# Kernel optimization log

Hardware: AMD Instinct MI355X
Metric: run time of the kernel (lower is better)

Reference implementation:

```python
import jax, jax.numpy as jnp
import numpy as np

B, T, C = 4, 2048, 1024
N_HEAD = 16
HEAD = C // N_HEAD

def setup_inputs() -> dict:
    key = jax.random.key(0)
    ks = jax.random.split(key, 5)
    return {
        "x": jax.random.normal(ks[0], (B, T, C), dtype=jnp.float32),
        "W_attn": jax.random.normal(ks[1], (C, 3 * C), dtype=jnp.float32) * (C ** -0.5),
        "b_attn": jax.random.normal(ks[2], (3 * C,), dtype=jnp.float32) * 0.02,
        "W_proj": jax.random.normal(ks[3], (C, C), dtype=jnp.float32) * (C ** -0.5),
        "b_proj": jax.random.normal(ks[4], (C,), dtype=jnp.float32) * 0.02,
    }

def reference(x, W_attn, b_attn, W_proj, b_proj):
    Bx, Tx, Cx = x.shape
    qkv = x @ W_attn + b_attn  # [B,T,3C]
    q, k, v = jnp.split(qkv, 3, axis=2)
    # [B,T,H,D] -> [B,H,T,D]
    q = q.reshape(Bx, Tx, N_HEAD, HEAD).transpose(0, 2, 1, 3)
    k = k.reshape(Bx, Tx, N_HEAD, HEAD).transpose(0, 2, 1, 3)
    v = v.reshape(Bx, Tx, N_HEAD, HEAD).transpose(0, 2, 1, 3)
    att = jnp.einsum('bhqd,bhkd->bhqk', q, k) * (HEAD ** -0.5)
    causal = jnp.tril(jnp.ones((Tx, Tx), dtype=bool))
    att = jnp.where(causal, att, jnp.float32(-jnp.inf))
    att = jax.nn.softmax(att, axis=-1)
    y = jnp.einsum('bhqk,bhkd->bhqd', att, v)
    y = y.transpose(0, 2, 1, 3).reshape(Bx, Tx, Cx)
    return y @ W_proj + b_proj
```

## Files before the change

kernel.cpp:

```cpp
#include <hip/hip_runtime.h>
#include <stdint.h>

#define NB 4
#define TT 2048
#define CC 1024
#define NH 16
#define DD 64
#define BHH (NB*NH)
#define MROWS (NB*TT)

typedef uint16_t u16;
typedef uint32_t u32;
typedef __bf16 bf16x8 __attribute__((ext_vector_type(8)));
typedef float f32x4 __attribute__((ext_vector_type(4)));
typedef float f32x16 __attribute__((ext_vector_type(16)));

__device__ __forceinline__ u16 f2bf(float f) {
    union { float f; uint32_t u; } v; v.f = f;
    uint32_t u = v.u;
    return (u16)((u + 0x7FFF + ((u >> 16) & 1)) >> 16);
}

__device__ __forceinline__ u32 cvtpk(float lo, float hi) {
    u32 r;
    asm volatile("v_cvt_pk_bf16_f32 %0, %1, %2" : "=v"(r) : "v"(lo), "v"(hi));
    return r;
}

__device__ __forceinline__ void plswap(u32& a, u32& b) {
    asm volatile("v_permlane32_swap_b32 %0, %1" : "+v"(a), "+v"(b));
}

__device__ __forceinline__ bf16x8 mk8(u32 a, u32 b, u32 c, u32 d) {
    union { u32 u[4]; bf16x8 v; } x;
    x.u[0] = a; x.u[1] = b; x.u[2] = c; x.u[3] = d;
    return x.v;
}

__device__ __forceinline__ void gl_lds16(const u16* g, u16* l) {
    __builtin_amdgcn_global_load_lds(
        (const __attribute__((address_space(1))) unsigned int*)g,
        (__attribute__((address_space(3))) unsigned int*)l, 16, 0, 0);
}

__device__ __forceinline__ f32x4 mfma16(bf16x8 a, bf16x8 b, f32x4 c) {
    return __builtin_amdgcn_mfma_f32_16x16x32_bf16(a, b, c, 0, 0, 0);
}
__device__ __forceinline__ f32x16 mfma32(bf16x8 a, bf16x8 b, f32x16 c) {
    return __builtin_amdgcn_mfma_f32_32x32x16_bf16(a, b, c, 0, 0, 0);
}

__global__ __launch_bounds__(256) void k_f2b(const float* __restrict__ in,
                                             u16* __restrict__ out, int n) {
    const int i = (blockIdx.x * 256 + threadIdx.x) * 4;
    if (i >= n) return;
    const float4 v = *(const float4*)(in + i);
    ushort4 o;
    o.x = f2bf(v.x); o.y = f2bf(v.y); o.z = f2bf(v.z); o.w = f2bf(v.w);
    *(ushort4*)(out + i) = o;
}

__global__ __launch_bounds__(256) void k_transpose_cvt(const float* __restrict__ in,
                                                       u16* __restrict__ out,
                                                       int R, int N) {
    __shared__ float t[32][33];
    const int n0 = blockIdx.x * 32, r0 = blockIdx.y * 32;
    const int c  = threadIdx.x & 31, rq = threadIdx.x >> 5;
#pragma unroll
    for (int i = 0; i < 4; ++i) {
        int r = rq + i * 8;
        t[r][c] = in[(r0 + r) * N + n0 + c];
    }
    __syncthreads();
#pragma unroll
    for (int i = 0; i < 4; ++i) {
        int r = rq + i * 8;
        out[(n0 + r) * R + r0 + c] = f2bf(t[c][r]);
    }
}

#define VM8()  do { asm volatile("s_waitcnt vmcnt(8)" ::: "memory"); \
                    __builtin_amdgcn_sched_barrier(0); } while (0)
#define VM0()  do { asm volatile("s_waitcnt vmcnt(0)" ::: "memory"); \
                    __builtin_amdgcn_sched_barrier(0); } while (0)

__device__ __forceinline__ void gemm128v4(const u16* __restrict__ A,
                                          const u16* __restrict__ Bt,
                                          int m0, int n0, f32x4 acc[4][4]) {
    __shared__ __align__(16) u16 As[2][128 * 64];
    __shared__ __align__(16) u16 Bs[2][128 * 64];
    const int tid = threadIdx.x, l = tid & 63, w = tid >> 6;
    const int wr = w >> 1, wc = w & 1;
    const int lr = l & 15, lg = l >> 4;

    auto stage = [&](int kt, int b) {
#pragma unroll
        for (int line = 0; line < 4; ++line) {
            const int s = line * 4096 + tid * 16;
            const int row = s >> 7;
            const int colb = (s & 127) ^ ((row & 7) << 4);
            const int ldsoff = (line * 4096 + w * 1024) >> 1;
            gl_lds16(A  + (size_t)(m0 + row) * 1024 + kt * 64 + (colb >> 1),
                     &As[b][ldsoff]);
            gl_lds16(Bt + (size_t)(n0 + row) * 1024 + kt * 64 + (colb >> 1),
                     &Bs[b][ldsoff]);
        }
    };

    stage(0, 0);
    stage(1, 1);
    VM8();
    __builtin_amdgcn_s_barrier();

    for (int kt = 0; kt < 16; ++kt) {
        const int b = kt & 1;

#pragma unroll
        for (int ks = 0; ks < 2; ++ks) {
            bf16x8 af[4], bf[4];
#pragma unroll
            for (int m = 0; m < 4; ++m) {
                const int row = wr * 64 + m * 16 + lr;
                const int byteC = (ks * 64 + lg * 16) ^ ((row & 7) << 4);
                af[m] = *(const bf16x8*)&As[b][(row * 128 + byteC) >> 1];
            }
#pragma unroll
            for (int n = 0; n < 4; ++n) {
                const int row = wc * 64 + n * 16 + lr;
                const int byteC = (ks * 64 + lg * 16) ^ ((row & 7) << 4);
                bf[n] = *(const bf16x8*)&Bs[b][(row * 128 + byteC) >> 1];
            }
#pragma unroll
            for (int m = 0; m < 4; ++m)
#pragma unroll
                for (int n = 0; n < 4; ++n)
                    acc[m][n] = mfma16(af[m], bf[n], acc[m][n]);
        }

        if (kt == 15) break;

        __builtin_amdgcn_s_barrier();

        if (kt + 2 < 16) {
            stage(kt + 2, b);
            VM8();
        } else {
            VM0();
        }
        __builtin_amdgcn_s_barrier();
    }
}

__global__ __launch_bounds__(256, 2) void k_gemm_qkv(const u16* __restrict__ X,
                                                     const u16* __restrict__ Wt,
                                                     const float* __restrict__ bias,
                                                     u16* __restrict__ Qo,
                                                     u16* __restrict__ Ko,
                                                     u16* __restrict__ Vto) {
    const int id = blockIdx.x;
    const int xcd = id & 7, lid = id >> 3;
    const int lm = lid & 7, ln = lid >> 3;
    const int m0 = (xcd * 8 + lm) * 128;
    const int n0 = ln * 128;

    f32x4 acc[4][4];
#pragma unroll
    for (int m = 0; m < 4; ++m)
#pragma unroll
        for (int n = 0; n < 4; ++n) acc[m][n] = (f32x4){0.f, 0.f, 0.f, 0.f};
    gemm128v4(X, Wt, m0, n0, acc);

    const float C2 = 0.18033688011112042f;
    const int tid = threadIdx.x, l = tid & 63, w = tid >> 6;
    const int wr = w >> 1, wc = w & 1, lr = l & 15, lg = l >> 4;
#pragma unroll
    for (int n = 0; n < 4; ++n) {
        const int c = n0 + wc * 64 + n * 16 + lr;
        const float bv = bias[c];
        const int which = c >> 10, cc = c & 1023, h = cc >> 6, d = cc & 63;
#pragma unroll
        for (int m = 0; m < 4; ++m) {
            const int rbase = m0 + wr * 64 + m * 16 + lg * 4;
#pragma unroll
            for (int j = 0; j < 4; ++j) {
                const int r = rbase + j;
                const int b = r >> 11, t = r & 2047;
                const int bh = b * NH + h;
                const float v = acc[m][n][j] + bv;
                if (which == 0)      Qo[(bh * TT + t) * DD + d] = f2bf(v * C2);
                else if (which == 1) Ko[(bh * TT + t) * DD + d] = f2bf(v);
                else                 Vto[(bh * DD + d) * TT + t] = f2bf(v);
            }
        }
    }
}

__global__ __launch_bounds__(256, 2) void k_gemm_proj(const u16* __restrict__ Yin,
                                                      const u16* __restrict__ Wt,
                                                      const float* __restrict__ bias,
                                                      float* __restrict__ out) {
    const int id = blockIdx.x;
    const int xcd = id & 7, lid = id >> 3;
    const int lm = lid & 7, ln = lid >> 3;
    const int m0 = (xcd * 8 + lm) * 128;
    const int n0 = ln * 128;

    f32x4 acc[4][4];
#pragma unroll
    for (int m = 0; m < 4; ++m)
#pragma unroll
        for (int n = 0; n < 4; ++n) acc[m][n] = (f32x4){0.f, 0.f, 0.f, 0.f};
    gemm128v4(Yin, Wt, m0, n0, acc);

    const int tid = threadIdx.x, l = tid & 63, w = tid >> 6;
    const int wr = w >> 1, wc = w & 1, lr = l & 15, lg = l >> 4;
#pragma unroll
    for (int n = 0; n < 4; ++n) {
        const int c = n0 + wc * 64 + n * 16 + lr;
        const float bv = bias[c];
#pragma unroll
        for (int m = 0; m < 4; ++m) {
            const int rbase = m0 + wr * 64 + m * 16 + lg * 4;
#pragma unroll
            for (int j = 0; j < 4; ++j) {
                const int r = rbase + j;
                out[r * CC + c] = acc[m][n][j] + bv;
            }
        }
    }
}

__global__ __launch_bounds__(256) void k_attn(const u16* __restrict__ Qg_,
                                              const u16* __restrict__ Kg_,
                                              const u16* __restrict__ Vg_,
                                              u16* __restrict__ Y) {
    __shared__ __align__(16) u16 Ks[2][64 * 64];
    __shared__ __align__(16) u16 Vs[2][64 * 64];

    const int id = blockIdx.x;
    const int qi = 15 - (id >> 6);
    const int bh = id & 63;
    const int q0 = qi * 128;
    const u16* Qg = Qg_ + (size_t)bh * TT * DD;
    const u16* Kg = Kg_ + (size_t)bh * TT * DD;
    const u16* Vg = Vg_ + (size_t)bh * DD * TT;
    const int tid = threadIdx.x, l = tid & 63, w = tid >> 6;
    const int lq = l & 31, hi = l >> 5;
    const int qs = q0 + w * 32;

    unsigned dmask = 0;
#pragma unroll
    for (int r = 0; r < 16; ++r) {
        const int kvloc = (r & 3) + 8 * (r >> 2) + 4 * hi;
        if (kvloc > lq) dmask |= (1u << r);
    }

    const u16* qrow = Qg + (qs + lq) * DD + hi * 8;
    bf16x8 qf0 = *(const bf16x8*)(qrow);
    bf16x8 qf1 = *(const bf16x8*)(qrow + 16);
    bf16x8 qf2 = *(const bf16x8*)(qrow + 32);
    bf16x8 qf3 = *(const bf16x8*)(qrow + 48);

    f32x16 o0 = {}, o1 = {};
    float mrun = -1e30f, lrun = 0.f;
    const int nt = 2 * qi + 2;

    auto stage = [&](int t, int b) {
        const int kv0 = t * 64;
#pragma unroll
        for (int iss = 0; iss < 2; ++iss) {
            const int s = iss * 4096 + tid * 16;
            const int row = s >> 7;
            const int colb = (s & 127) ^ ((row & 7) << 4);
            const int ldsoff = (iss * 4096 + w * 1024) >> 1;
            gl_lds16(Kg + (kv0 + row) * DD + (colb >> 1), &Ks[b][ldsoff]);
            gl_lds16(Vg + row * TT + kv0 + (colb >> 1),   &Vs[b][ldsoff]);
        }
    };

    stage(0, 0);
    __syncthreads();

    for (int t = 0; t < nt; ++t) {
        const int b = t & 1;
        if (t + 1 < nt) stage(t + 1, b ^ 1);
        const int kv0 = t * 64;

#pragma unroll
        for (int s = 0; s < 2; ++s) {
            const int kvs = kv0 + 32 * s;
            if (kvs > qs) continue;

            f32x16 st = {};
#pragma unroll
            for (int i = 0; i < 4; ++i) {
                const int row = 32 * s + lq;
                const int byte = (32 * i + 16 * hi) ^ ((row & 7) << 4);
                const bf16x8 kf = *(const bf16x8*)&Ks[b][(row * 128 + byte) >> 1];
                if (i == 0) st = mfma32(kf, qf0, st);
                else if (i == 1) st = mfma32(kf, qf1, st);
                else if (i == 2) st = mfma32(kf, qf2, st);
                else st = mfma32(kf, qf3, st);
            }

            if (kvs == qs) {
#pragma unroll
                for (int r = 0; r < 16; ++r)
                    if ((dmask >> r) & 1) st[r] = -1e30f;
            }

            float mx = st[0];
#pragma unroll
            for (int r = 1; r < 16; ++r) mx = fmaxf(mx, st[r]);
            mx = fmaxf(mx, __shfl_xor(mx, 32));

            if (!__all(mx - mrun <= 8.0f)) {
                const float mn = fmaxf(mrun, mx);
                const float scl = __builtin_amdgcn_exp2f(mrun - mn);
                mrun = mn;
                lrun *= scl;
#pragma unroll
                for (int r = 0; r < 16; ++r) { o0[r] *= scl; o1[r] *= scl; }
            }

            float psum = 0.f;
            u32 pk0, pk1, pk2, pk3, pk4, pk5, pk6, pk7;
            {
                float pa, pb;
                pa = __builtin_amdgcn_exp2f(st[0] - mrun);
                pb = __builtin_amdgcn_exp2f(st[1] - mrun);
                psum += pa + pb; pk0 = cvtpk(pa, pb);
                pa = __builtin_amdgcn_exp2f(st[2] - mrun);
                pb = __builtin_amdgcn_exp2f(st[3] - mrun);
                psum += pa + pb; pk1 = cvtpk(pa, pb);
                pa = __builtin_amdgcn_exp2f(st[4] - mrun);
                pb = __builtin_amdgcn_exp2f(st[5] - mrun);
                psum += pa + pb; pk2 = cvtpk(pa, pb);
                pa = __builtin_amdgcn_exp2f(st[6] - mrun);
                pb = __builtin_amdgcn_exp2f(st[7] - mrun);
                psum += pa + pb; pk3 = cvtpk(pa, pb);
                pa = __builtin_amdgcn_exp2f(st[8] - mrun);
                pb = __builtin_amdgcn_exp2f(st[9] - mrun);
                psum += pa + pb; pk4 = cvtpk(pa, pb);
                pa = __builtin_amdgcn_exp2f(st[10] - mrun);
                pb = __builtin_amdgcn_exp2f(st[11] - mrun);
                psum += pa + pb; pk5 = cvtpk(pa, pb);
                pa = __builtin_amdgcn_exp2f(st[12] - mrun);
                pb = __builtin_amdgcn_exp2f(st[13] - mrun);
                psum += pa + pb; pk6 = cvtpk(pa, pb);
                pa = __builtin_amdgcn_exp2f(st[14] - mrun);
                pb = __builtin_amdgcn_exp2f(st[15] - mrun);
                psum += pa + pb; pk7 = cvtpk(pa, pb);
            }
            lrun += psum;

            plswap(pk0, pk2); plswap(pk1, pk3);
            plswap(pk4, pk6); plswap(pk5, pk7);
            const bf16x8 pf0 = mk8(pk0, pk1, pk2, pk3);
            const bf16x8 pf1 = mk8(pk4, pk5, pk6, pk7);

#pragma unroll
            for (int dh = 0; dh < 2; ++dh) {
#pragma unroll
                for (int ks = 0; ks < 2; ++ks) {
                    const int row = 32 * dh + lq;
                    const int byte = (64 * s + 32 * ks + 16 * hi) ^ ((row & 7) << 4);
                    const bf16x8 vf = *(const bf16x8*)&Vs[b][(row * 128 + byte) >> 1];
                    if (dh == 0) o0 = mfma32(vf, ks ? pf1 : pf0, o0);
                    else         o1 = mfma32(vf, ks ? pf1 : pf0, o1);
                }
            }
        }
        if (t + 1 < nt) __syncthreads();
    }

    lrun += __shfl_xor(lrun, 32);
    const float inv = 1.0f / lrun;
    const int bb = bh >> 4, h = bh & 15;
    u16* yrow = Y + (size_t)(bb * TT + qs + lq) * CC + h * DD;
#pragma unroll
    for (int rq = 0; rq < 4; ++rq) {
        const int d0 = 8 * rq + 4 * hi;
        const u32 w0 = cvtpk(o0[rq * 4 + 0] * inv, o0[rq * 4 + 1] * inv);
        const u32 w1 = cvtpk(o0[rq * 4 + 2] * inv, o0[rq * 4 + 3] * inv);
        *(uint2*)&yrow[d0] = make_uint2(w0, w1);
        const u32 w2 = cvtpk(o1[rq * 4 + 0] * inv, o1[rq * 4 + 1] * inv);
        const u32 w3 = cvtpk(o1[rq * 4 + 2] * inv, o1[rq * 4 + 3] * inv);
        *(uint2*)&yrow[32 + d0] = make_uint2(w2, w3);
    }
}

extern "C" void kernel_launch(void* const* d_in, const int* in_sizes, int n_in,
                              void* d_out, int out_size, void* d_ws, size_t ws_size,
                              hipStream_t stream) {
    const float* X  = (const float*)d_in[0];
    const float* Wa = (const float*)d_in[1];
    const float* ba = (const float*)d_in[2];
    const float* Wp = (const float*)d_in[3];
    const float* bp = (const float*)d_in[4];
    float* out = (float*)d_out;

    u16* ws  = (u16*)d_ws;
    u16* Xb  = ws;
    u16* WtA = Xb + (size_t)MROWS * CC;
    u16* WtP = WtA + 3072 * 1024;
    u16* Qb  = WtP + 1024 * 1024;
    u16* Kb  = Qb + (size_t)BHH * TT * DD;
    u16* Vtb = Kb + (size_t)BHH * TT * DD;
    u16* Yb  = Vtb + (size_t)BHH * TT * DD;

    k_f2b<<<dim3(MROWS * CC / 1024), 256, 0, stream>>>(X, Xb, MROWS * CC);
    k_transpose_cvt<<<dim3(96, 32), 256, 0, stream>>>(Wa, WtA, 1024, 3072);
    k_transpose_cvt<<<dim3(32, 32), 256, 0, stream>>>(Wp, WtP, 1024, 1024);
    k_gemm_qkv<<<dim3(1536), 256, 0, stream>>>(Xb, WtA, ba, Qb, Kb, Vtb);
    k_attn<<<dim3(1024), 256, 0, stream>>>(Qb, Kb, Vtb, Yb);
    k_gemm_proj<<<dim3(512), 256, 0, stream>>>(Yb, WtP, bp, out);
}
```

Measured before the change: 178.2 us.

## Use 128x256 tiles with BK=32 for the QKV projection GEMM

```diff
diff --git a/kernel.cpp b/kernel.cpp
--- a/kernel.cpp
+++ b/kernel.cpp
@@ -49,6 +49,13 @@
 __device__ __forceinline__ f32x16 mfma32(bf16x8 a, bf16x8 b, f32x16 c) {
     return __builtin_amdgcn_mfma_f32_32x32x16_bf16(a, b, c, 0, 0, 0);
 }
+
+#define VM6()  do { asm volatile("s_waitcnt vmcnt(6)" ::: "memory"); \
+                    __builtin_amdgcn_sched_barrier(0); } while (0)
+#define VM8()  do { asm volatile("s_waitcnt vmcnt(8)" ::: "memory"); \
+                    __builtin_amdgcn_sched_barrier(0); } while (0)
+#define VM0()  do { asm volatile("s_waitcnt vmcnt(0)" ::: "memory"); \
+                    __builtin_amdgcn_sched_barrier(0); } while (0)
 
 __global__ __launch_bounds__(256) void k_f2b(const float* __restrict__ in,
                                              u16* __restrict__ out, int n) {
@@ -79,10 +86,121 @@
     }
 }
 
-#define VM8()  do { asm volatile("s_waitcnt vmcnt(8)" ::: "memory"); \
-                    __builtin_amdgcn_sched_barrier(0); } while (0)
-#define VM0()  do { asm volatile("s_waitcnt vmcnt(0)" ::: "memory"); \
-                    __builtin_amdgcn_sched_barrier(0); } while (0)
+__device__ __forceinline__ void gemm128x256(const u16* __restrict__ A,
+                                            const u16* __restrict__ Bt,
+                                            int m0, int n0, f32x4 acc[4][8]) {
+    __shared__ __align__(16) u16 As[2][128 * 32];
+    __shared__ __align__(16) u16 Bs[2][256 * 32];
+    const int tid = threadIdx.x, l = tid & 63, w = tid >> 6;
+    const int wr = w >> 1, wc = w & 1;
+    const int lr = l & 15, lg = l >> 4;
+
+    auto stage = [&](int kt, int b) {
+#pragma unroll
+        for (int line = 0; line < 2; ++line) {
+            const int s = line * 4096 + tid * 16;
+            const int row = s >> 6;
+            const int colb = (s & 63) ^ (((row >> 1) & 3) << 4);
+            gl_lds16(A + (size_t)(m0 + row) * 1024 + kt * 32 + (colb >> 1),
+                     &As[b][(line * 4096 + w * 1024) >> 1]);
+        }
+#pragma unroll
+        for (int line = 0; line < 4; ++line) {
+            const int s = line * 4096 + tid * 16;
+            const int row = s >> 6;
+            const int colb = (s & 63) ^ (((row >> 1) & 3) << 4);
+            gl_lds16(Bt + (size_t)(n0 + row) * 1024 + kt * 32 + (colb >> 1),
+                     &Bs[b][(line * 4096 + w * 1024) >> 1]);
+        }
+    };
+
+    stage(0, 0);
+    stage(1, 1);
+    VM6();
+    __builtin_amdgcn_s_barrier();
+
+    for (int kt = 0; kt < 32; ++kt) {
+        const int b = kt & 1;
+
+        bf16x8 af[4];
+#pragma unroll
+        for (int m = 0; m < 4; ++m) {
+            const int row = wr * 64 + m * 16 + lr;
+            const int byteC = (lg * 16) ^ (((row >> 1) & 3) << 4);
+            af[m] = *(const bf16x8*)&As[b][(row * 64 + byteC) >> 1];
+        }
+#pragma unroll
+        for (int nh = 0; nh < 2; ++nh) {
+            bf16x8 bf[4];
+#pragma unroll
+            for (int n = 0; n < 4; ++n) {
+                const int row = wc * 128 + nh * 64 + n * 16 + lr;
+                const int byteC = (lg * 16) ^ (((row >> 1) & 3) << 4);
+                bf[n] = *(const bf16x8*)&Bs[b][(row * 64 + byteC) >> 1];
+            }
+#pragma unroll
+            for (int m = 0; m < 4; ++m)
+#pragma unroll
+                for (int n = 0; n < 4; ++n)
+                    acc[m][nh * 4 + n] = mfma16(af[m], bf[n], acc[m][nh * 4 + n]);
+        }
+
+        if (kt == 31) break;
+
+        __builtin_amdgcn_s_barrier();
+        if (kt + 2 < 32) {
+            stage(kt + 2, b);
+            VM6();
+        } else {
+            VM0();
+        }
+        __builtin_amdgcn_s_barrier();
+    }
+}
+
+__global__ __launch_bounds__(256, 3) void k_gemm_qkv(const u16* __restrict__ X,
+                                                     const u16* __restrict__ Wt,
+                                                     const float* __restrict__ bias,
+                                                     u16* __restrict__ Qo,
+                                                     u16* __restrict__ Ko,
+                                                     u16* __restrict__ Vto) {
+    const int id = blockIdx.x;
+    const int xcd = id & 7, lid = id >> 3;
+    const int lm = lid & 7, ln = lid >> 3;
+    const int m0 = (xcd * 8 + lm) * 128;
+    const int n0 = ln * 256;
+
+    f32x4 acc[4][8];
+#pragma unroll
+    for (int m = 0; m < 4; ++m)
+#pragma unroll
+        for (int n = 0; n < 8; ++n) acc[m][n] = (f32x4){0.f, 0.f, 0.f, 0.f};
+    gemm128x256(X, Wt, m0, n0, acc);
+
+    const float C2 = 0.18033688011112042f;
+    const int tid = threadIdx.x, l = tid & 63, w = tid >> 6;
+    const int wr = w >> 1, wc = w & 1, lr = l & 15, lg = l >> 4;
+#pragma unroll
+    for (int nf = 0; nf < 8; ++nf) {
+        const int c = n0 + wc * 128 + nf * 16 + lr;
+        const float bv = bias[c];
+        const int which = c >> 10, cc = c & 1023, h = cc >> 6, d = cc & 63;
+#pragma unroll
+        for (int mf = 0; mf < 4; ++mf) {
+            const int rbase = m0 + wr * 64 + mf * 16 + lg * 4;
+#pragma unroll
+            for (int j = 0; j < 4; ++j) {
+                const int r = rbase + j;
+                const int b = r >> 11, t = r & 2047;
+                const int bh = b * NH + h;
+                const float v = acc[mf][nf][j] + bv;
+                if (which == 0)      Qo[(bh * TT + t) * DD + d] = f2bf(v * C2);
+                else if (which == 1) Ko[(bh * TT + t) * DD + d] = f2bf(v);
+                else                 Vto[(bh * DD + d) * TT + t] = f2bf(v);
+            }
+        }
+    }
+}
 
 __device__ __forceinline__ void gemm128v4(const u16* __restrict__ A,
                                           const u16* __restrict__ Bt,
@@ -114,7 +232,6 @@
 
     for (int kt = 0; kt < 16; ++kt) {
         const int b = kt & 1;
-
 #pragma unroll
         for (int ks = 0; ks < 2; ++ks) {
             bf16x8 af[4], bf[4];
@@ -138,9 +255,7 @@
         }
 
         if (kt == 15) break;
-
         __builtin_amdgcn_s_barrier();
-
         if (kt + 2 < 16) {
             stage(kt + 2, b);
             VM8();
@@ -148,50 +263,6 @@
             VM0();
         }
         __builtin_amdgcn_s_barrier();
-    }
-}
-
-__global__ __launch_bounds__(256, 2) void k_gemm_qkv(const u16* __restrict__ X,
-                                                     const u16* __restrict__ Wt,
-                                                     const float* __restrict__ bias,
-                                                     u16* __restrict__ Qo,
-                                                     u16* __restrict__ Ko,
-                                                     u16* __restrict__ Vto) {
-    const int id = blockIdx.x;
-    const int xcd = id & 7, lid = id >> 3;
-    const int lm = lid & 7, ln = lid >> 3;
-    const int m0 = (xcd * 8 + lm) * 128;
-    const int n0 = ln * 128;
-
-    f32x4 acc[4][4];
-#pragma unroll
-    for (int m = 0; m < 4; ++m)
-#pragma unroll
-        for (int n = 0; n < 4; ++n) acc[m][n] = (f32x4){0.f, 0.f, 0.f, 0.f};
-    gemm128v4(X, Wt, m0, n0, acc);
-
-    const float C2 = 0.18033688011112042f;
-    const int tid = threadIdx.x, l = tid & 63, w = tid >> 6;
-    const int wr = w >> 1, wc = w & 1, lr = l & 15, lg = l >> 4;
-#pragma unroll
-    for (int n = 0; n < 4; ++n) {
-        const int c = n0 + wc * 64 + n * 16 + lr;
-        const float bv = bias[c];
-        const int which = c >> 10, cc = c & 1023, h = cc >> 6, d = cc & 63;
-#pragma unroll
-        for (int m = 0; m < 4; ++m) {
-            const int rbase = m0 + wr * 64 + m * 16 + lg * 4;
-#pragma unroll
-            for (int j = 0; j < 4; ++j) {
-                const int r = rbase + j;
-                const int b = r >> 11, t = r & 2047;
-                const int bh = b * NH + h;
-                const float v = acc[m][n][j] + bv;
-                if (which == 0)      Qo[(bh * TT + t) * DD + d] = f2bf(v * C2);
-                else if (which == 1) Ko[(bh * TT + t) * DD + d] = f2bf(v);
-                else                 Vto[(bh * DD + d) * TT + t] = f2bf(v);
-            }
-        }
     }
 }
 
@@ -412,7 +483,7 @@
     k_f2b<<<dim3(MROWS * CC / 1024), 256, 0, stream>>>(X, Xb, MROWS * CC);
     k_transpose_cvt<<<dim3(96, 32), 256, 0, stream>>>(Wa, WtA, 1024, 3072);
     k_transpose_cvt<<<dim3(32, 32), 256, 0, stream>>>(Wp, WtP, 1024, 1024);
-    k_gemm_qkv<<<dim3(1536), 256, 0, stream>>>(Xb, WtA, ba, Qb, Kb, Vtb);
+    k_gemm_qkv<<<dim3(768), 256, 0, stream>>>(Xb, WtA, ba, Qb, Kb, Vtb);
     k_attn<<<dim3(1024), 256, 0, stream>>>(Qb, Kb, Vtb, Yb);
     k_gemm_proj<<<dim3(512), 256, 0, stream>>>(Yb, WtP, bp, out);
 }
```

Result: slower. 226.1 us (+26.9%).
